# Kernel optimization log

Measured on AMD Instinct MI355X. Metric: run time of the kernel, lower is better.

## Reference

```python
import jax, jax.numpy as jnp
import numpy as np

N = 100000   # nodes
E = 600000   # edges per graph
F = 512      # node_features == input_size
H = 256      # n_hidden
H2 = 128     # n_hidden // 2
O = 1        # output_size
EPS = 1e-5


def gcn_conv(x, W, b, src, dst, n):
    # PyG GCNConv: add self-loops, symmetric normalization, then scatter-add.
    xw = x @ W                                   # [N, out]
    loop = jnp.arange(n)
    s = jnp.concatenate([src, loop])
    d = jnp.concatenate([dst, loop])
    deg = jax.ops.segment_sum(jnp.ones_like(d, jnp.float32), d, num_segments=n)
    dis = jnp.where(deg > 0, jax.lax.rsqrt(jnp.maximum(deg, 1.0)), 0.0)
    norm = dis[s] * dis[d]                       # [E+N]
    msg = xw[s] * norm[:, None]
    return jax.ops.segment_sum(msg, d, num_segments=n) + b


def sage_conv(x, Wl, bl, Wr, src, dst, n):
    # PyG SAGEConv (mean aggr): lin_l(mean_neigh) + lin_r(x); lin_r has no bias.
    agg = jax.ops.segment_sum(x[src], dst, num_segments=n)
    cnt = jax.ops.segment_sum(jnp.ones_like(dst, jnp.float32), dst, num_segments=n)
    mean = agg / jnp.maximum(cnt, 1.0)[:, None]
    return mean @ Wl + bl + x @ Wr


def layer_norm(x, w, b):
    mu = jnp.mean(x, axis=-1, keepdims=True)
    var = jnp.mean(jnp.square(x - mu), axis=-1, keepdims=True)
    return (x - mu) * jax.lax.rsqrt(var + EPS) * w + b


def mlp(x, Wm1, bm1, ln_w, ln_b, Wm2, bm2):
    h = layer_norm(x @ Wm1 + bm1, ln_w, ln_b)
    return h @ Wm2 + bm2


def setup_inputs() -> dict:
    key = jax.random.key(0)
    ks = jax.random.split(key, 22)
    s = 0.05
    d = {}
    d["x"] = jax.random.normal(ks[0], (N, F), jnp.float32)
    d["x1"] = jax.random.normal(ks[1], (N, F), jnp.float32)
    d["edge_index"] = jax.random.randint(ks[2], (2, E), 0, N)
    d["edge_index1"] = jax.random.randint(ks[3], (2, E), 0, N)
    # conv1_1 / conv2_1: GCNConv(F -> H)
    d["Wg1"] = jax.random.normal(ks[4], (F, H), jnp.float32) * s
    d["bg1"] = jnp.zeros((H,), jnp.float32)
    d["Wg2"] = jax.random.normal(ks[5], (F, H), jnp.float32) * s
    d["bg2"] = jnp.zeros((H,), jnp.float32)
    # conv1_2 / conv2_2: SAGEConv(H -> H2)
    d["Wl1"] = jax.random.normal(ks[6], (H, H2), jnp.float32) * s
    d["bl1"] = jnp.zeros((H2,), jnp.float32)
    d["Wr1"] = jax.random.normal(ks[7], (H, H2), jnp.float32) * s
    d["Wl2"] = jax.random.normal(ks[8], (H, H2), jnp.float32) * s
    d["bl2"] = jnp.zeros((H2,), jnp.float32)
    d["Wr2"] = jax.random.normal(ks[9], (H, H2), jnp.float32) * s
    # shared MLP: Linear(H2,H2) -> LayerNorm(H2) -> Linear(H2,O)
    d["Wm1"] = jax.random.normal(ks[10], (H2, H2), jnp.float32) * s
    d["bm1"] = jnp.zeros((H2,), jnp.float32)
    d["ln_w"] = jnp.ones((H2,), jnp.float32)
    d["ln_b"] = jnp.zeros((H2,), jnp.float32)
    d["Wm2"] = jax.random.normal(ks[11], (H2, O), jnp.float32) * s
    d["bm2"] = jnp.zeros((O,), jnp.float32)
    return d


def reference(x, x1, edge_index, edge_index1, Wg1, bg1, Wg2, bg2,
              Wl1, bl1, Wr1, Wl2, bl2, Wr2, Wm1, bm1, ln_w, ln_b, Wm2, bm2):
    src, dst = edge_index[0], edge_index[1]
    src1, dst1 = edge_index1[0], edge_index1[1]
    n = x.shape[0]

    h = gcn_conv(x, Wg1, bg1, src, dst, n)
    h0 = jax.nn.relu(h)                          # x0 = relu(conv1_1)
    g = gcn_conv(x1, Wg2, bg2, src1, dst1, n)
    g0 = jax.nn.relu(g)                          # x1_0 = relu(conv2_1)

    x0 = h0 + g0
    a = jax.nn.relu(sage_conv(x0, Wl1, bl1, Wr1, src, dst, n))
    a = mlp(a, Wm1, bm1, ln_w, ln_b, Wm2, bm2)   # [N, 1]
    a = jnp.squeeze(a)                            # [N]

    g1 = g0 + g                                   # x1_0 + x1 (pre-relu conv2_1)
    b_ = jax.nn.relu(sage_conv(g1, Wl2, bl2, Wr2, src1, dst1, n))
    b_ = mlp(b_, Wm1, bm1, ln_w, ln_b, Wm2, bm2)
    b_ = jnp.squeeze(b_)                          # [N]

    cat = jnp.concatenate([a, b_], axis=0)        # [2N]
    out = jnp.mean(cat)
    return out[None, None]                        # [1, 1]
```

## Files before the change

### kernel.cpp

```cpp
#include <hip/hip_runtime.h>

#define NN 100000
#define EE 600000
#define FF 512
#define HH 256
#define HD2 128

typedef unsigned short u16;
typedef unsigned int u32;
typedef __attribute__((ext_vector_type(4))) float f32x4;
typedef __attribute__((ext_vector_type(8))) short bf16x8;

__device__ __forceinline__ float bflo(u32 u){ return __uint_as_float(u << 16); }
__device__ __forceinline__ float bfhi(u32 u){ return __uint_as_float(u & 0xffff0000u); }
__device__ __forceinline__ u32 f2bf(float x){
  u32 u = __float_as_uint(x);
  return (u + 0x7FFFu + ((u >> 16) & 1u)) >> 16;
}
__device__ __forceinline__ u32 pack2(float x, float y){ return f2bf(x) | (f2bf(y) << 16); }

__global__ void zero_int_k(int* __restrict__ p, int n){
  int i = blockIdx.x * 256 + threadIdx.x;
  int st = gridDim.x * 256;
  for (; i < n; i += st) p[i] = 0;
}

__global__ void count_deg_k(const int* __restrict__ dst, int* __restrict__ deg, int nE){
  int e = blockIdx.x * 256 + threadIdx.x;
  if (e < nE) atomicAdd(&deg[dst[e]], 1);
}

__global__ __launch_bounds__(256) void scan1_k(const int* __restrict__ deg, int* __restrict__ out,
                                               int* __restrict__ aux, int n){
  __shared__ int sm[256];
  const int t = threadIdx.x;
  const int base = blockIdx.x * 1024 + t * 4;
  int v0 = (base+0) < n ? deg[base+0] : 0;
  int v1 = (base+1) < n ? deg[base+1] : 0;
  int v2 = (base+2) < n ? deg[base+2] : 0;
  int v3 = (base+3) < n ? deg[base+3] : 0;
  int s = v0 + v1 + v2 + v3;
  sm[t] = s;
  __syncthreads();
  for (int off = 1; off < 256; off <<= 1){
    int x = (t >= off) ? sm[t - off] : 0;
    __syncthreads();
    sm[t] += x;
    __syncthreads();
  }
  if (t == 255) aux[blockIdx.x] = sm[255];
  int run = sm[t] - s;
  if (base+0 < n) out[base+0] = run;            run += v0;
  if (base+1 < n) out[base+1] = run;            run += v1;
  if (base+2 < n) out[base+2] = run;            run += v2;
  if (base+3 < n) out[base+3] = run;
}
__global__ void scan2_k(int* __restrict__ aux, int nchunks){
  if (threadIdx.x == 0){
    int run = 0;
    for (int i = 0; i < nchunks; ++i){ int t = aux[i]; aux[i] = run; run += t; }
  }
}
__global__ void scan3_k(int* __restrict__ out, const int* __restrict__ aux, int n){
  int i = blockIdx.x * 256 + threadIdx.x;
  if (i < n) out[i] += aux[i >> 10];
}

__global__ void csr_fill_k(const int* __restrict__ src, const int* __restrict__ dst,
                           const int* __restrict__ rp, int* __restrict__ fill,
                           int* __restrict__ csr, int nE){
  int e = blockIdx.x * 256 + threadIdx.x;
  if (e >= nE) return;
  int d = dst[e];
  int pos = rp[d] + atomicAdd(&fill[d], 1);
  csr[pos] = src[e];
}

__global__ void wtcvt_k(const float* __restrict__ W, u16* __restrict__ WT,
                        int K, int nmask, int nshift, int total){
  int idx = blockIdx.x * 256 + threadIdx.x;
  if (idx >= total) return;
  int k = idx >> nshift, n = idx & nmask;
  WT[(size_t)n * K + k] = (u16)f2bf(W[idx]);
}

__global__ __launch_bounds__(256) void gemm_xw_k(
    const float* __restrict__ A, const u16* __restrict__ BT,
    u16* __restrict__ C, int M)
{
  __shared__ u16 As[128][40];
  __shared__ u16 Bs[128][40];
  const int tid = threadIdx.x;
  const int w = tid >> 6, lane = tid & 63;
  const int row0 = blockIdx.x * 128, col0 = blockIdx.y * 128;
  const int wr = (w >> 1) * 64, wc = (w & 1) * 64;
  const int sar = tid >> 1, sak = (tid & 1) * 16;
  const int lrow = lane & 15, lk = (lane >> 4) * 8;
  f32x4 acc[4][4];
#pragma unroll
  for (int i = 0; i < 4; ++i)
#pragma unroll
    for (int j = 0; j < 4; ++j)
#pragma unroll
      for (int q = 0; q < 4; ++q) acc[i][j][q] = 0.f;

  const bool aval = (row0 + sar) < M;
  const float* apb = A + (size_t)(row0 + sar) * FF + sak;

  for (int kb = 0; kb < FF; kb += 32){
    if (aval){
      const float4* ap = (const float4*)(apb + kb);
      float4 v0 = ap[0], v1 = ap[1], v2 = ap[2], v3 = ap[3];
      uint4 p0 = make_uint4(pack2(v0.x,v0.y), pack2(v0.z,v0.w), pack2(v1.x,v1.y), pack2(v1.z,v1.w));
      uint4 p1 = make_uint4(pack2(v2.x,v2.y), pack2(v2.z,v2.w), pack2(v3.x,v3.y), pack2(v3.z,v3.w));
      *(uint4*)&As[sar][sak]     = p0;
      *(uint4*)&As[sar][sak + 8] = p1;
    } else {
      uint4 z = make_uint4(0,0,0,0);
      *(uint4*)&As[sar][sak]     = z;
      *(uint4*)&As[sar][sak + 8] = z;
    }
    for (int c = tid; c < 512; c += 256){
      int n = c >> 2, part = c & 3;
      uint4 bv = *(const uint4*)(BT + (size_t)(col0 + n) * FF + kb + part * 8);
      *(uint4*)&Bs[n][part * 8] = bv;
    }
    __syncthreads();
    bf16x8 af[4], bfr[4];
#pragma unroll
    for (int mt = 0; mt < 4; ++mt) af[mt]  = *(const bf16x8*)&As[wr + mt*16 + lrow][lk];
#pragma unroll
    for (int nt = 0; nt < 4; ++nt) bfr[nt] = *(const bf16x8*)&Bs[wc + nt*16 + lrow][lk];
#pragma unroll
    for (int mt = 0; mt < 4; ++mt)
#pragma unroll
      for (int nt = 0; nt < 4; ++nt)
        acc[mt][nt] = __builtin_amdgcn_mfma_f32_16x16x32_bf16(af[mt], bfr[nt], acc[mt][nt], 0, 0, 0);
    __syncthreads();
  }
  const int orow = (lane >> 4) * 4, ocol = lane & 15;
#pragma unroll
  for (int mt = 0; mt < 4; ++mt)
#pragma unroll
    for (int i = 0; i < 4; ++i){
      int r = row0 + wr + mt*16 + orow + i;
      if (r < M){
        u16* cp = C + (size_t)r * HH + col0 + wc + ocol;
#pragma unroll
        for (int nt = 0; nt < 4; ++nt)
          cp[nt * 16] = (u16)f2bf(acc[mt][nt][i]);
      }
    }
}

__global__ __launch_bounds__(256) void gcn_agg_k(
    const u16* __restrict__ XW, const int* __restrict__ rp,
    const int* __restrict__ deg, const int* __restrict__ csr,
    const float* __restrict__ bias, u16* __restrict__ H, int n)
{
  const int d = blockIdx.x * 4 + (threadIdx.x >> 6);
  if (d >= n) return;
  const int lane = threadIdx.x & 63;
  const int dg = deg[d];
  const float disd = rsqrtf((float)dg + 1.0f);
  const uint2* xw2 = (const uint2*)XW;
  uint2 sv = xw2[(size_t)d * 64 + lane];
  const float sw = disd * disd;
  float a0 = bflo(sv.x) * sw, a1 = bfhi(sv.x) * sw;
  float a2 = bflo(sv.y) * sw, a3 = bfhi(sv.y) * sw;
  const int s0 = rp[d], s1 = s0 + dg;
  for (int i = s0; i < s1; ++i){
    int s = csr[i];
    float wgt = rsqrtf((float)deg[s] + 1.0f) * disd;
    uint2 v = xw2[(size_t)s * 64 + lane];
    a0 = fmaf(bflo(v.x), wgt, a0); a1 = fmaf(bfhi(v.x), wgt, a1);
    a2 = fmaf(bflo(v.y), wgt, a2); a3 = fmaf(bfhi(v.y), wgt, a3);
  }
  const float4 bv = *(const float4*)(bias + lane * 4);
  a0 += bv.x; a1 += bv.y; a2 += bv.z; a3 += bv.w;
  uint2 o; o.x = pack2(a0, a1); o.y = pack2(a2, a3);
  ((uint2*)H)[(size_t)d * 64 + lane] = o;
}

__global__ __launch_bounds__(256) void sage_mean_k(
    const u16* __restrict__ X, const int* __restrict__ rp,
    const int* __restrict__ deg, const int* __restrict__ csr,
    u16* __restrict__ Mo, int n)
{
  const int d = blockIdx.x * 4 + (threadIdx.x >> 6);
  if (d >= n) return;
  const int lane = threadIdx.x & 63;
  const int dg = deg[d];
  const uint2* x2 = (const uint2*)X;
  float a0 = 0.f, a1 = 0.f, a2 = 0.f, a3 = 0.f;
  const int s0 = rp[d], s1 = s0 + dg;
  for (int i = s0; i < s1; ++i){
    int s = csr[i];
    uint2 v = x2[(size_t)s * 64 + lane];
    a0 += bflo(v.x); a1 += bfhi(v.x);
    a2 += bflo(v.y); a3 += bfhi(v.y);
  }
  const float sc = 1.0f / (float)(dg > 0 ? dg : 1);
  uint2 o; o.x = pack2(a0 * sc, a1 * sc); o.y = pack2(a2 * sc, a3 * sc);
  ((uint2*)Mo)[(size_t)d * 64 + lane] = o;
}

__global__ void combine_k(u32* __restrict__ X0, u32* __restrict__ G1,
                          const u32* __restrict__ H1, const u32* __restrict__ H2)
{
  int i = blockIdx.x * 256 + threadIdx.x;
  u32 uh = H1[i], ug = H2[i];
  float h0 = bflo(uh), h1 = bfhi(uh), g0 = bflo(ug), g1 = bfhi(ug);
  float rh0 = fmaxf(h0, 0.f), rh1 = fmaxf(h1, 0.f);
  float rg0 = fmaxf(g0, 0.f), rg1 = fmaxf(g1, 0.f);
  X0[i] = pack2(rh0 + rg0, rh1 + rg1);
  G1[i] = pack2(rg0 + g0, rg1 + g1);
}

__global__ __launch_bounds__(256) void sage_gemm_k(
    const u16* __restrict__ A1, const u16* __restrict__ A2,
    const u16* __restrict__ B1T, const u16* __restrict__ B2T,
    const float* __restrict__ bias, u16* __restrict__ S, int M)
{
  __shared__ u16 As[128][40];
  __shared__ u16 Bs[128][40];
  const int tid = threadIdx.x;
  const int w = tid >> 6, lane = tid & 63;
  const int row0 = blockIdx.x * 128;
  const int wr = (w >> 1) * 64, wc = (w & 1) * 64;
  const int lrow = lane & 15, lk = (lane >> 4) * 8;
  f32x4 acc[4][4];
#pragma unroll
  for (int i = 0; i < 4; ++i)
#pragma unroll
    for (int j = 0; j < 4; ++j)
#pragma unroll
      for (int q = 0; q < 4; ++q) acc[i][j][q] = 0.f;

  for (int pass = 0; pass < 2; ++pass){
    const u16* Ap = pass ? A2 : A1;
    const u16* Bp = pass ? B2T : B1T;
    for (int kb = 0; kb < HH; kb += 32){
      for (int c = tid; c < 512; c += 256){
        int r = c >> 2, part = c & 3;
        int grow = row0 + r;
        uint4 v = make_uint4(0,0,0,0);
        if (grow < M) v = *(const uint4*)(Ap + (size_t)grow * HH + kb + part * 8);
        *(uint4*)&As[r][part * 8] = v;
      }
      for (int c = tid; c < 512; c += 256){
        int n = c >> 2, part = c & 3;
        uint4 v = *(const uint4*)(Bp + (size_t)n * HH + kb + part * 8);
        *(uint4*)&Bs[n][part * 8] = v;
      }
      __syncthreads();
      bf16x8 af[4], bfr[4];
#pragma unroll
      for (int mt = 0; mt < 4; ++mt) af[mt]  = *(const bf16x8*)&As[wr + mt*16 + lrow][lk];
#pragma unroll
      for (int nt = 0; nt < 4; ++nt) bfr[nt] = *(const bf16x8*)&Bs[wc + nt*16 + lrow][lk];
#pragma unroll
      for (int mt = 0; mt < 4; ++mt)
#pragma unroll
        for (int nt = 0; nt < 4; ++nt)
          acc[mt][nt] = __builtin_amdgcn_mfma_f32_16x16x32_bf16(af[mt], bfr[nt], acc[mt][nt], 0, 0, 0);
      __syncthreads();
    }
  }
  const int orow = (lane >> 4) * 4, ocol = lane & 15;
#pragma unroll
  for (int mt = 0; mt < 4; ++mt)
#pragma unroll
    for (int i = 0; i < 4; ++i){
      int r = row0 + wr + mt*16 + orow + i;
      if (r < M){
        u16* cp = S + (size_t)r * HD2 + wc + ocol;
#pragma unroll
        for (int nt = 0; nt < 4; ++nt){
          float v = acc[mt][nt][i] + bias[wc + nt*16 + ocol];
          cp[nt * 16] = (u16)f2bf(fmaxf(v, 0.f));
        }
      }
    }
}

__global__ __launch_bounds__(256) void mlp_mfma_k(
    const u16* __restrict__ Xin,
    const u16* __restrict__ W1T,
    const float* __restrict__ bm1,
    const float* __restrict__ lnw, const float* __restrict__ lnb,
    const float* __restrict__ Wm2, const float* __restrict__ bm2,
    double* __restrict__ partial, int M)
{
  __shared__ u16 Wsh[HD2][136];
  __shared__ double wsum[4];
  const int tid = threadIdx.x;
  const int lane = tid & 63, wv = tid >> 6;
  const int g = lane >> 4, cn = lane & 15;

  for (int i = tid; i < HD2 * 16; i += 256){
    int j = i >> 4, c = i & 15;
    *(uint4*)&Wsh[j][c * 8] = ((const uint4*)W1T)[i];
  }

  f32x4 b1v[8], c1v[8];
  float S1 = 0.f, C0 = 0.f;
#pragma unroll
  for (int jt = 0; jt < 8; ++jt){
    int j = jt * 16 + g * 4;
    float4 bb = *(const float4*)&bm1[j];
    float4 lw = *(const float4*)&lnw[j];
    float4 lb = *(const float4*)&lnb[j];
    float4 w2 = *(const float4*)&Wm2[j];
    b1v[jt][0] = bb.x; b1v[jt][1] = bb.y; b1v[jt][2] = bb.z; b1v[jt][3] = bb.w;
    c1v[jt][0] = lw.x * w2.x; c1v[jt][1] = lw.y * w2.y;
    c1v[jt][2] = lw.z * w2.z; c1v[jt][3] = lw.w * w2.w;
    S1 += c1v[jt][0] + c1v[jt][1] + c1v[jt][2] + c1v[jt][3];
    C0 += lb.x * w2.x + lb.y * w2.y + lb.z * w2.z + lb.w * w2.w;
  }
  S1 += __shfl_xor(S1, 16); S1 += __shfl_xor(S1, 32);
  C0 += __shfl_xor(C0, 16); C0 += __shfl_xor(C0, 32);
  const float bm2v = bm2[0];
  __syncthreads();

  double local = 0.0;
  const int stride = gridDim.x * 64;
  for (int base = blockIdx.x * 64 + wv * 16; base < M; base += stride){
    const int node = base + cn;
    const bool nv = node < M;
    f32x4 acc[8];
#pragma unroll
    for (int jt = 0; jt < 8; ++jt){ acc[jt][0]=0.f; acc[jt][1]=0.f; acc[jt][2]=0.f; acc[jt][3]=0.f; }
#pragma unroll
    for (int ks = 0; ks < 4; ++ks){
      bf16x8 bfv = {0,0,0,0,0,0,0,0};
      if (nv) bfv = *(const bf16x8*)(Xin + (size_t)node * HD2 + ks * 32 + g * 8);
#pragma unroll
      for (int jt = 0; jt < 8; ++jt){
        bf16x8 afr = *(const bf16x8*)&Wsh[jt * 16 + cn][ks * 32 + g * 8];
        acc[jt] = __builtin_amdgcn_mfma_f32_16x16x32_bf16(afr, bfv, acc[jt], 0, 0, 0);
      }
    }
    float s = 0.f;
#pragma unroll
    for (int jt = 0; jt < 8; ++jt){
#pragma unroll
      for (int r = 0; r < 4; ++r){
        acc[jt][r] += b1v[jt][r];
        s += acc[jt][r];
      }
    }
    s += __shfl_xor(s, 16); s += __shfl_xor(s, 32);
    const float mu = s * (1.0f / HD2);
    float vs = 0.f, d1 = 0.f;
#pragma unroll
    for (int jt = 0; jt < 8; ++jt){
#pragma unroll
      for (int r = 0; r < 4; ++r){
        float dv = acc[jt][r] - mu;
        vs = fmaf(dv, dv, vs);
        d1 = fmaf(acc[jt][r], c1v[jt][r], d1);
      }
    }
    vs += __shfl_xor(vs, 16); vs += __shfl_xor(vs, 32);
    d1 += __shfl_xor(d1, 16); d1 += __shfl_xor(d1, 32);
    const float rs = rsqrtf(vs * (1.0f / HD2) + 1e-5f);
    const float p = rs * (d1 - mu * S1) + C0 + bm2v;
    if (nv && g == 0) local += (double)p;
  }
#pragma unroll
  for (int off = 32; off > 0; off >>= 1) local += __shfl_xor(local, off);
  if (lane == 0) wsum[wv] = local;
  __syncthreads();
  if (tid == 0) partial[blockIdx.x] = wsum[0] + wsum[1] + wsum[2] + wsum[3];
}

__global__ __launch_bounds__(256) void final_reduce_k(
    const double* __restrict__ P, u32* __restrict__ out)
{
  __shared__ double sm[256];
  const int tid = threadIdx.x;
  double s = P[tid] + P[tid + 256] + P[tid + 512] + P[tid + 768];
  sm[tid] = s;
  __syncthreads();
  for (int h = 128; h > 0; h >>= 1){
    if (tid < h) sm[tid] += sm[tid + h];
    __syncthreads();
  }
  if (tid == 0){
    float v = (float)(sm[0] * (1.0 / (2.0 * (double)NN)));
    u32 bf = f2bf(v);
    out[0] = (bf << 16) | bf;
  }
}

extern "C" void kernel_launch(void* const* d_in, const int* in_sizes, int n_in,
                              void* d_out, int out_size, void* d_ws, size_t ws_size,
                              hipStream_t stream)
{
  const float* x   = (const float*)d_in[0];
  const float* x1  = (const float*)d_in[1];
  const int* ei  = (const int*)d_in[2];
  const int* ei1 = (const int*)d_in[3];
  const float* Wg1 = (const float*)d_in[4];
  const float* bg1 = (const float*)d_in[5];
  const float* Wg2 = (const float*)d_in[6];
  const float* bg2 = (const float*)d_in[7];
  const float* Wl1 = (const float*)d_in[8];
  const float* bl1 = (const float*)d_in[9];
  const float* Wr1 = (const float*)d_in[10];
  const float* Wl2 = (const float*)d_in[11];
  const float* bl2 = (const float*)d_in[12];
  const float* Wr2 = (const float*)d_in[13];
  const float* Wm1 = (const float*)d_in[14];
  const float* bm1 = (const float*)d_in[15];
  const float* lnw = (const float*)d_in[16];
  const float* lnb = (const float*)d_in[17];
  const float* Wm2 = (const float*)d_in[18];
  const float* bm2 = (const float*)d_in[19];

  const int* src1 = ei,  * dst1 = ei + EE;
  const int* src2 = ei1, * dst2 = ei1 + EE;

  u16* U0 = (u16*)d_ws;
  u16* U1 = U0 + (size_t)NN * HH;
  u16* U2 = U1 + (size_t)NN * HH;
  u16* U3 = U2 + (size_t)NN * HH;
  u16* U4 = U3 + (size_t)NN * HH;
  u16* U5 = U4 + (size_t)NN * HD2;
  u16* WG1T = U5 + (size_t)NN * HD2;
  u16* WG2T = WG1T + HH * FF;
  u16* WL1T = WG2T + HH * FF;
  u16* WR1T = WL1T + HD2 * HH;
  u16* WL2T = WR1T + HD2 * HH;
  u16* WR2T = WL2T + HD2 * HH;
  int* deg1 = (int*)(WR2T + HD2 * HH);
  int* deg2 = deg1 + NN;
  int* fill1 = deg2 + NN;
  int* fill2 = fill1 + NN;
  int* rp1 = fill2 + NN;
  int* rp2 = rp1 + NN;
  int* aux1 = rp2 + NN;
  int* aux2 = aux1 + 128;
  int* csr1 = aux2 + 128;
  int* csr2 = csr1 + EE;
  double* P = (double*)(csr2 + EE);
  u16* WM1T = U0;

  const int eblk = (EE + 255) / 256;
  const int nchunks = (NN + 1023) / 1024;

  zero_int_k<<<512, 256, 0, stream>>>(deg1, 4 * NN);
  count_deg_k<<<eblk, 256, 0, stream>>>(dst1, deg1, EE);
  count_deg_k<<<eblk, 256, 0, stream>>>(dst2, deg2, EE);
  scan1_k<<<nchunks, 256, 0, stream>>>(deg1, rp1, aux1, NN);
  scan1_k<<<nchunks, 256, 0, stream>>>(deg2, rp2, aux2, NN);
  scan2_k<<<1, 64, 0, stream>>>(aux1, nchunks);
  scan2_k<<<1, 64, 0, stream>>>(aux2, nchunks);
  scan3_k<<<(NN + 255) / 256, 256, 0, stream>>>(rp1, aux1, NN);
  scan3_k<<<(NN + 255) / 256, 256, 0, stream>>>(rp2, aux2, NN);
  csr_fill_k<<<eblk, 256, 0, stream>>>(src1, dst1, rp1, fill1, csr1, EE);
  csr_fill_k<<<eblk, 256, 0, stream>>>(src2, dst2, rp2, fill2, csr2, EE);

  wtcvt_k<<<512, 256, 0, stream>>>(Wg1, WG1T, FF, HH - 1, 8, FF * HH);
  wtcvt_k<<<512, 256, 0, stream>>>(Wg2, WG2T, FF, HH - 1, 8, FF * HH);
  wtcvt_k<<<128, 256, 0, stream>>>(Wl1, WL1T, HH, HD2 - 1, 7, HH * HD2);
  wtcvt_k<<<128, 256, 0, stream>>>(Wr1, WR1T, HH, HD2 - 1, 7, HH * HD2);
  wtcvt_k<<<128, 256, 0, stream>>>(Wl2, WL2T, HH, HD2 - 1, 7, HH * HD2);
  wtcvt_k<<<128, 256, 0, stream>>>(Wr2, WR2T, HH, HD2 - 1, 7, HH * HD2);

  dim3 ggrid((NN + 127) / 128, HH / 128);
  gemm_xw_k<<<ggrid, 256, 0, stream>>>(x,  WG1T, U0, NN);
  gemm_xw_k<<<ggrid, 256, 0, stream>>>(x1, WG2T, U1, NN);

  gcn_agg_k<<<NN / 4, 256, 0, stream>>>(U0, rp1, deg1, csr1, bg1, U2, NN);
  gcn_agg_k<<<NN / 4, 256, 0, stream>>>(U1, rp2, deg2, csr2, bg2, U3, NN);

  combine_k<<<NN * HH / 512, 256, 0, stream>>>((u32*)U0, (u32*)U1, (const u32*)U2, (const u32*)U3);

  sage_mean_k<<<NN / 4, 256, 0, stream>>>(U0, rp1, deg1, csr1, U2, NN);
  sage_mean_k<<<NN / 4, 256, 0, stream>>>(U1, rp2, deg2, csr2, U3, NN);

  sage_gemm_k<<<(NN + 127) / 128, 256, 0, stream>>>(U2, U0, WL1T, WR1T, bl1, U4, NN);
  sage_gemm_k<<<(NN + 127) / 128, 256, 0, stream>>>(U3, U1, WL2T, WR2T, bl2, U5, NN);

  wtcvt_k<<<64, 256, 0, stream>>>(Wm1, WM1T, HD2, HD2 - 1, 7, HD2 * HD2);

  mlp_mfma_k<<<1024, 256, 0, stream>>>(U4, WM1T, bm1, lnw, lnb, Wm2, bm2, P, 2 * NN);

  final_reduce_k<<<1, 256, 0, stream>>>(P, (u32*)d_out);
}
```

Baseline: 1.265 ms.

## Double-buffer XW GEMM with direct global-to-LDS loads and swizzled layout

Rewrites the X@W GEMM main loop to stage A (fp32) and B tiles through double-buffered LDS using global_load_lds, so the next K-slice load overlaps MFMA compute on the current one. The fp32-to-bf16 conversion moves from the global-load path to after the LDS read, using the hardware packed-convert instruction. An XOR swizzle replaces the padded layout to avoid bank conflicts. Staging A as fp32 doubles its LDS footprint and read traffic. Rows past M are clamped rather than zeroed, and the extra barrier waits add some synchronisation cost.

Result: faster. 1.234 ms (-2.4%).

```diff
diff --git a/kernel.cpp b/kernel.cpp
--- a/kernel.cpp
+++ b/kernel.cpp
@@ -10,6 +10,7 @@
 typedef unsigned int u32;
 typedef __attribute__((ext_vector_type(4))) float f32x4;
 typedef __attribute__((ext_vector_type(8))) short bf16x8;
+typedef __attribute__((ext_vector_type(4))) unsigned int u32x4;
 
 __device__ __forceinline__ float bflo(u32 u){ return __uint_as_float(u << 16); }
 __device__ __forceinline__ float bfhi(u32 u){ return __uint_as_float(u & 0xffff0000u); }
@@ -18,6 +19,16 @@
   return (u + 0x7FFFu + ((u >> 16) & 1u)) >> 16;
 }
 __device__ __forceinline__ u32 pack2(float x, float y){ return f2bf(x) | (f2bf(y) << 16); }
+
+__device__ __forceinline__ void gll16(const void* g, void* l){
+  __builtin_amdgcn_global_load_lds((const __attribute__((address_space(1))) void*)g,
+                                   (__attribute__((address_space(3))) void*)l, 16, 0, 0);
+}
+__device__ __forceinline__ u32 cvtpk(float lo, float hi){
+  u32 r;
+  asm("v_cvt_pk_bf16_f32 %0, %1, %2" : "=v"(r) : "v"(lo), "v"(hi));
+  return r;
+}
 
 __global__ void zero_int_k(int* __restrict__ p, int n){
   int i = blockIdx.x * 256 + threadIdx.x;
@@ -88,14 +99,36 @@
     const float* __restrict__ A, const u16* __restrict__ BT,
     u16* __restrict__ C, int M)
 {
-  __shared__ u16 As[128][40];
-  __shared__ u16 Bs[128][40];
+  __shared__ float As[2][4096];
+  __shared__ u16  Bs[2][4096];
   const int tid = threadIdx.x;
   const int w = tid >> 6, lane = tid & 63;
   const int row0 = blockIdx.x * 128, col0 = blockIdx.y * 128;
   const int wr = (w >> 1) * 64, wc = (w & 1) * 64;
-  const int sar = tid >> 1, sak = (tid & 1) * 16;
-  const int lrow = lane & 15, lk = (lane >> 4) * 8;
+  const int lrow = lane & 15, g = lane >> 4;
+
+  u32 aoff[4], alds[4];
+#pragma unroll
+  for (int i = 0; i < 4; ++i){
+    int S = (w * 4 + i) * 64 + lane;
+    int L = S ^ ((S >> 3) & 7);
+    int r = L >> 3, c = L & 7;
+    int rr = row0 + r; if (rr > M - 1) rr = M - 1;
+    aoff[i] = (u32)rr * (FF * 4u) + (u32)c * 16u;
+    alds[i] = (u32)(w * 4 + i) * 1024u;
+  }
+  u32 boff[2], blds[2];
+#pragma unroll
+  for (int i = 0; i < 2; ++i){
+    int S = (w * 2 + i) * 64 + lane;
+    int L = S ^ ((S >> 3) & 7);
+    int col = L >> 2, cb = L & 3;
+    boff[i] = (u32)(col0 + col) * (FF * 2u) + (u32)cb * 16u;
+    blds[i] = (u32)(w * 2 + i) * 1024u;
+  }
+  const char* Ab = (const char*)A;
+  const char* Bb = (const char*)BT;
+
   f32x4 acc[4][4];
 #pragma unroll
   for (int i = 0; i < 4; ++i)
@@ -104,46 +137,60 @@
 #pragma unroll
       for (int q = 0; q < 4; ++q) acc[i][j][q] = 0.f;
 
-  const bool aval = (row0 + sar) < M;
-  const float* apb = A + (size_t)(row0 + sar) * FF + sak;
-
-  for (int kb = 0; kb < FF; kb += 32){
-    if (aval){
-      const float4* ap = (const float4*)(apb + kb);
-      float4 v0 = ap[0], v1 = ap[1], v2 = ap[2], v3 = ap[3];
-      uint4 p0 = make_uint4(pack2(v0.x,v0.y), pack2(v0.z,v0.w), pack2(v1.x,v1.y), pack2(v1.z,v1.w));
-      uint4 p1 = make_uint4(pack2(v2.x,v2.y), pack2(v2.z,v2.w), pack2(v3.x,v3.y), pack2(v3.z,v3.w));
-      *(uint4*)&As[sar][sak]     = p0;
-      *(uint4*)&As[sar][sak + 8] = p1;
-    } else {
-      uint4 z = make_uint4(0,0,0,0);
-      *(uint4*)&As[sar][sak]     = z;
-      *(uint4*)&As[sar][sak + 8] = z;
-    }
-    for (int c = tid; c < 512; c += 256){
-      int n = c >> 2, part = c & 3;
-      uint4 bv = *(const uint4*)(BT + (size_t)(col0 + n) * FF + kb + part * 8);
-      *(uint4*)&Bs[n][part * 8] = bv;
-    }
-    __syncthreads();
+#pragma unroll
+  for (int i = 0; i < 4; ++i) gll16(Ab + aoff[i], (char*)&As[0][0] + alds[i]);
+#pragma unroll
+  for (int i = 0; i < 2; ++i) gll16(Bb + boff[i], (char*)&Bs[0][0] + blds[i]);
+  asm volatile("s_waitcnt vmcnt(0)" ::: "memory");
+  __builtin_amdgcn_s_barrier();
+
+  for (int t = 0; t < FF / 32; ++t){
+    const int cur = t & 1, nxt = cur ^ 1;
+    if (t < FF / 32 - 1){
+      const int kb = (t + 1) * 32;
+#pragma unroll
+      for (int i = 0; i < 4; ++i) gll16(Ab + aoff[i] + kb * 4, (char*)&As[nxt][0] + alds[i]);
+#pragma unroll
+      for (int i = 0; i < 2; ++i) gll16(Bb + boff[i] + kb * 2, (char*)&Bs[nxt][0] + blds[i]);
+    }
+    const char* Ac = (const char*)&As[cur][0];
+    const char* Bc = (const char*)&Bs[cur][0];
     bf16x8 af[4], bfr[4];
 #pragma unroll
-    for (int mt = 0; mt < 4; ++mt) af[mt]  = *(const bf16x8*)&As[wr + mt*16 + lrow][lk];
-#pragma unroll
-    for (int nt = 0; nt < 4; ++nt) bfr[nt] = *(const bf16x8*)&Bs[wc + nt*16 + lrow][lk];
+    for (int nt = 0; nt < 4; ++nt){
+      int col = wc + nt * 16 + lrow;
+      int S = (col * 4 + g) ^ ((col >> 1) & 7);
+      bfr[nt] = *(const bf16x8*)(Bc + S * 16);
+    }
+#pragma unroll
+    for (int mt = 0; mt < 4; ++mt){
+      int r = wr + mt * 16 + lrow;
+      int S0 = r * 8 + ((2 * g)     ^ (r & 7));
+      int S1 = r * 8 + ((2 * g + 1) ^ (r & 7));
+      f32x4 fa = *(const f32x4*)(Ac + S0 * 16);
+      f32x4 fb = *(const f32x4*)(Ac + S1 * 16);
+      u32x4 q;
+      q.x = cvtpk(fa[0], fa[1]);
+      q.y = cvtpk(fa[2], fa[3]);
+      q.z = cvtpk(fb[0], fb[1]);
+      q.w = cvtpk(fb[2], fb[3]);
+      af[mt] = __builtin_bit_cast(bf16x8, q);
+    }
 #pragma unroll
     for (int mt = 0; mt < 4; ++mt)
 #pragma unroll
       for (int nt = 0; nt < 4; ++nt)
         acc[mt][nt] = __builtin_amdgcn_mfma_f32_16x16x32_bf16(af[mt], bfr[nt], acc[mt][nt], 0, 0, 0);
-    __syncthreads();
-  }
+    asm volatile("s_waitcnt vmcnt(0)" ::: "memory");
+    __builtin_amdgcn_s_barrier();
+  }
+
   const int orow = (lane >> 4) * 4, ocol = lane & 15;
 #pragma unroll
   for (int mt = 0; mt < 4; ++mt)
 #pragma unroll
     for (int i = 0; i < 4; ++i){
-      int r = row0 + wr + mt*16 + orow + i;
+      int r = row0 + wr + mt * 16 + orow + i;
       if (r < M){
         u16* cp = C + (size_t)r * HH + col0 + wc + ocol;
 #pragma unroll
```
